# Optimization experiments

Hardware: AMD Instinct MI355X
Metric: run time of the kernel (lower is better)

Reference implementation:

```python
import jax, jax.numpy as jnp
import numpy as np

D = 1024          # embeddings_dims
HS = 128          # head_size = D // no_of_q_heads(=8)
NKV = 2           # hardcoded self.no_of_kv_heads = 2 (number of query Linear layers)


def apply_rope(x):
    # x: [..., T, d]; pairs of adjacent elements rotated (faithful to RotaryEmbeddings)
    d = x.shape[-1]
    T = x.shape[-2]
    positions = jnp.arange(0, d, 2, dtype=jnp.float32)           # step-2 positions (as in source)
    theta = 10000.0 ** (-2.0 * positions / d)                    # [d/2]
    angles = jnp.arange(T, dtype=jnp.float32)[:, None] * theta[None, :]  # [T, d/2]
    cos, sin = jnp.cos(angles), jnp.sin(angles)
    xr = x.reshape(x.shape[:-1] + (d // 2, 2))
    out = jnp.stack([xr[..., 0] * cos - xr[..., 1] * sin,
                     xr[..., 1] * cos + xr[..., 0] * sin], axis=-1)
    return out.reshape(x.shape)


def setup_inputs() -> dict:
    key = jax.random.key(0)
    k1, k2, k3, k4, k5 = jax.random.split(key, 5)
    B, T = 4, 2048
    x = jax.random.normal(k1, (B, T, D), dtype=jnp.float32)
    s = 1.0 / np.sqrt(D)
    Wq = jax.random.normal(k2, (NKV, HS, D), dtype=jnp.float32) * s  # 2 query Linear layers [out,in]
    Wk = jax.random.normal(k3, (HS, D), dtype=jnp.float32) * s
    Wv = jax.random.normal(k4, (HS, D), dtype=jnp.float32) * s
    Wo = jax.random.normal(k5, (D, NKV * HS), dtype=jnp.float32) * (1.0 / np.sqrt(NKV * HS))
    return {"x": x, "Wq": Wq, "Wk": Wk, "Wv": Wv, "Wo": Wo}


def reference(x, Wq, Wk, Wv, Wo):
    B, T, _ = x.shape
    k = apply_rope(x @ Wk.T)                              # [B,T,HS]
    v = x @ Wv.T                                          # [B,T,HS]
    q = jnp.einsum('btd,hkd->bhtk', x, Wq)                # [B,2,T,HS]
    q = apply_rope(q)
    scale = HS ** (-0.5)
    scores = jnp.einsum('bhtk,bsk->bhts', q, k) * scale   # [B,2,T,T]
    causal = jnp.tril(jnp.ones((T, T), dtype=bool))
    scores = jnp.where(causal, scores, -jnp.inf)
    w = jax.nn.softmax(scores, axis=-1)                   # dropout is identity at eval
    out = jnp.einsum('bhts,bsk->bhtk', w, v)              # [B,2,T,HS]
    out = out.transpose(0, 2, 1, 3).reshape(B, T, NKV * HS)  # concat heads on last dim
    return out @ Wo.T                                     # [B,T,D]
```

## Files before the change

### kernel.cpp

```cpp
#include <hip/hip_runtime.h>
#include <math.h>

#define DD 1024
#define HSZ 128
#define NB 4
#define TT 2048

typedef __attribute__((ext_vector_type(8))) short bf16x8;
typedef __attribute__((ext_vector_type(4))) float f32x4;

typedef __attribute__((address_space(3))) unsigned int lds_u32_t;
typedef __attribute__((address_space(1))) unsigned int glb_u32_t;

__device__ inline void gll16(const void* g, void* l) {
    __builtin_amdgcn_global_load_lds((const glb_u32_t*)g, (lds_u32_t*)l, 16, 0, 0);
}

__device__ inline unsigned short f2bf(float f){
    unsigned u = __builtin_bit_cast(unsigned, f);
    u += 0x7fff + ((u >> 16) & 1);
    return (unsigned short)(u >> 16);
}

__global__ __launch_bounds__(256) void prep_kernel(
    const float* __restrict__ Wq, const float* __restrict__ Wk,
    const float* __restrict__ Wv, const float* __restrict__ Wo,
    unsigned short* __restrict__ Wbp, unsigned short* __restrict__ Wop,
    float2* __restrict__ tab)
{
    int bid = blockIdx.x, tid = threadIdx.x;
    if (bid < 512) {
        int i = bid * 256 + tid;
        int t = i >> 6, j = i & 63;
        float theta = __powf(10000.f, -(float)j * (1.f / 32.f));
        float ang = (float)t * theta;
        tab[i] = make_float2(__cosf(ang), __sinf(ang));
        return;
    }
    const float* s;
    unsigned short* dst;
    if (bid < 768) {
        int gc = (bid - 512) * 256 + tid;
        int tileid = gc >> 10;
        int ct = tileid >> 4, kk = tileid & 15;
        int ch = gc & 1023;
        int ns = ch >> 7, kc = (ch >> 6) & 1, l6 = ch & 63;
        int wrow = ct * 128 + ns * 16 + (l6 & 15);
        int kcol = kk * 64 + kc * 32 + (l6 >> 4) * 8;
        s = (wrow < 256) ? Wq + (size_t)wrow * DD
          : (wrow < 384) ? Wk + (size_t)(wrow - 256) * DD
                         : Wv + (size_t)(wrow - 384) * DD;
        s += kcol;
        dst = Wbp + (size_t)gc * 8;
    } else {
        int gc = (bid - 768) * 256 + tid;
        int tileid = gc >> 10;
        int ct = tileid >> 2, kk = tileid & 3;
        int ch = gc & 1023;
        int ns = ch >> 7, kc = (ch >> 6) & 1, l6 = ch & 63;
        int orow = ct * 128 + ns * 16 + (l6 & 15);
        int kcol = kk * 64 + kc * 32 + (l6 >> 4) * 8;
        s = Wo + (size_t)orow * 256 + kcol;
        dst = Wop + (size_t)gc * 8;
    }
    float4 a = ((const float4*)s)[0];
    float4 c = ((const float4*)s)[1];
    unsigned short o[8] = {f2bf(a.x),f2bf(a.y),f2bf(a.z),f2bf(a.w),
                           f2bf(c.x),f2bf(c.y),f2bf(c.z),f2bf(c.w)};
    *(uint4*)dst = *(const uint4*)o;
}

__global__ __launch_bounds__(256) void qkv_gemm_kernel(
    const float* __restrict__ x,
    const unsigned short* __restrict__ Wbp,
    const float2* __restrict__ tab,
    unsigned short* __restrict__ qo,
    unsigned short* __restrict__ Kp,
    unsigned short* __restrict__ Vp)
{
    int bid = blockIdx.x;
    int rt = bid & 127, ct = bid >> 7;
    int row0 = rt * 64;
    int b = row0 >> 11, t0 = row0 & (TT - 1);
    int tid = threadIdx.x;
    int wave = tid >> 6, lane = tid & 63;
    int mrow = lane & 15, quad = lane >> 4;

    __shared__ unsigned short Bs[2][8192];

    f32x4 acc[8];
    #pragma unroll
    for (int ns = 0; ns < 8; ++ns)
        #pragma unroll
        for (int r = 0; r < 4; ++r) acc[ns][r] = 0.f;

    const float* xrow = x + (size_t)(row0 + wave * 16 + mrow) * DD;

    {
        const unsigned short* wt = Wbp + (size_t)(ct * 16) * 8192;
        #pragma unroll
        for (int u = 0; u < 4; ++u)
            gll16(wt + (size_t)(u * 256 + tid) * 8, &Bs[0][(u * 256 + (tid & 192)) * 8]);
    }

    for (int kk = 0; kk < 16; ++kk) {
        __syncthreads();
        if (kk < 15) {
            const unsigned short* wt = Wbp + (size_t)(ct * 16 + kk + 1) * 8192;
            #pragma unroll
            for (int u = 0; u < 4; ++u)
                gll16(wt + (size_t)(u * 256 + tid) * 8, &Bs[(kk + 1) & 1][(u * 256 + (tid & 192)) * 8]);
        }
        bf16x8 af[2];
        #pragma unroll
        for (int kc = 0; kc < 2; ++kc) {
            const float* s = xrow + kk * 64 + kc * 32 + quad * 8;
            float4 f0 = ((const float4*)s)[0];
            float4 f1 = ((const float4*)s)[1];
            bf16x8 pk;
            pk[0]=(short)f2bf(f0.x); pk[1]=(short)f2bf(f0.y); pk[2]=(short)f2bf(f0.z); pk[3]=(short)f2bf(f0.w);
            pk[4]=(short)f2bf(f1.x); pk[5]=(short)f2bf(f1.y); pk[6]=(short)f2bf(f1.z); pk[7]=(short)f2bf(f1.w);
            af[kc] = pk;
        }
        const unsigned short* Bcur = Bs[kk & 1];
        #pragma unroll
        for (int kc = 0; kc < 2; ++kc)
            #pragma unroll
            for (int ns = 0; ns < 8; ++ns) {
                bf16x8 bb = *(const bf16x8*)(Bcur + ((ns * 2 + kc) * 64 + lane) * 8);
                acc[ns] = __builtin_amdgcn_mfma_f32_16x16x32_bf16(af[kc], bb, acc[ns], 0, 0, 0);
            }
    }

    __syncthreads();

    if (ct < 2) {
        unsigned short* dst = qo + (size_t)(b * 2 + ct) * TT * HSZ;
        #pragma unroll
        for (int ns = 0; ns < 8; ++ns) {
            int colloc = ns * 16 + mrow;
            int pj = colloc >> 1;
            #pragma unroll
            for (int r = 0; r < 4; ++r) {
                int t = t0 + wave * 16 + quad * 4 + r;
                float v = acc[ns][r];
                float vp = __shfl_xor(v, 1, 64);
                float2 cs = tab[t * 64 + pj];
                float outv = ((mrow & 1) == 0) ? (v * cs.x - vp * cs.y)
                                               : (v * cs.x + vp * cs.y);
                dst[(size_t)t * HSZ + colloc] = f2bf(outv);
            }
        }
    } else if (ct == 2) {
        unsigned short* A_ = (unsigned short*)Bs;
        #pragma unroll
        for (int ns = 0; ns < 8; ++ns) {
            int colloc = ns * 16 + mrow;
            int pj = colloc >> 1;
            int chunk = (ns >> 1) * 4 + wave;
            int lph = (ns & 1) * 2 + (mrow >> 3);
            #pragma unroll
            for (int r = 0; r < 4; ++r) {
                int t = t0 + wave * 16 + quad * 4 + r;
                float v = acc[ns][r];
                float vp = __shfl_xor(v, 1, 64);
                float2 cs = tab[t * 64 + pj];
                float outv = ((mrow & 1) == 0) ? (v * cs.x - vp * cs.y)
                                               : (v * cs.x + vp * cs.y);
                A_[chunk * 512 + (lph * 16 + quad * 4 + r) * 8 + (mrow & 7)] = f2bf(outv);
            }
        }
        __syncthreads();
        unsigned short* kd = Kp + (size_t)(b * 32 + (t0 >> 6)) * 8192;
        #pragma unroll
        for (int u = 0; u < 4; ++u)
            *(uint4*)(kd + (u * 256 + tid) * 8) = *(const uint4*)(A_ + (u * 256 + tid) * 8);
    } else {
        unsigned short* A_ = (unsigned short*)Bs;
        #pragma unroll
        for (int ns = 0; ns < 8; ++ns) {
            int chunk = ns * 2 + (wave >> 1);
            int lanep = ((wave & 1) * 2 + (quad >> 1)) * 16 + mrow;
            #pragma unroll
            for (int r = 0; r < 4; ++r)
                A_[chunk * 512 + lanep * 8 + (quad & 1) * 4 + r] = f2bf(acc[ns][r]);
        }
        __syncthreads();
        unsigned short* vd = Vp + (size_t)(b * 32 + (t0 >> 6)) * 8192;
        #pragma unroll
        for (int u = 0; u < 4; ++u)
            *(uint4*)(vd + (u * 256 + tid) * 8) = *(const uint4*)(A_ + (u * 256 + tid) * 8);
    }
}

__global__ __launch_bounds__(256, 2) void attn_mfma_kernel(
    const unsigned short* __restrict__ q,
    const unsigned short* __restrict__ Kp,
    const unsigned short* __restrict__ Vp,
    unsigned short* __restrict__ att)
{
    int bid = blockIdx.x;
    int qt = 63 - (bid >> 3);
    int bh = bid & 7;
    int b = bh >> 1, h = bh & 1;
    int q0 = qt * 32;
    int tid = threadIdx.x;
    int wave = tid >> 6, lane = tid & 63;
    int mrow = lane & 15, quad = lane >> 4;

    __shared__ char raw[66304];
    unsigned short* Psb = (unsigned short*)raw;
    float* Os  = (float*)(raw + 16384);
    float* Ms_ = (float*)(raw + 65536);
    float* Ls_ = Ms_ + 96;

    const unsigned short* qbase = q + (((size_t)(b * 2 + h)) * TT + q0 + mrow) * HSZ + quad * 8;
    bf16x8 qf[2][4];
    #pragma unroll
    for (int u = 0; u < 2; ++u)
        #pragma unroll
        for (int c = 0; c < 4; ++c)
            qf[u][c] = *(const bf16x8*)(qbase + u * 16 * HSZ + 32 * c);

    float mrun[2][4], lrun[2][4];
    f32x4 O[2][8];
    #pragma unroll
    for (int u = 0; u < 2; ++u) {
        #pragma unroll
        for (int r = 0; r < 4; ++r) { mrun[u][r] = -1e30f; lrun[u][r] = 0.f; }
        #pragma unroll
        for (int g = 0; g < 8; ++g)
            #pragma unroll
            for (int r = 0; r < 4; ++r) O[u][g][r] = 0.f;
    }

    const int NT = (qt >> 1) + 1;
    const float scl = 0.08838834764831845f;
    unsigned short* Pw = Psb + wave * 2048;

    for (int j = wave; j < NT; j += 4) {
        const unsigned short* Kt = Kp + (size_t)(b * 32 + j) * 8192;
        const unsigned short* Vt = Vp + (size_t)(b * 32 + j) * 8192;
        int s0 = j * 64;

        f32x4 S[2][4];
        #pragma unroll
        for (int u = 0; u < 2; ++u)
            #pragma unroll
            for (int f = 0; f < 4; ++f)
                #pragma unroll
                for (int r = 0; r < 4; ++r) S[u][f][r] = 0.f;

        #pragma unroll
        for (int c = 0; c < 4; ++c)
            #pragma unroll
            for (int f = 0; f < 4; ++f) {
                bf16x8 bk = *(const bf16x8*)(Kt + ((c * 4 + f) * 64 + lane) * 8);
                S[0][f] = __builtin_amdgcn_mfma_f32_16x16x32_bf16(qf[0][c], bk, S[0][f], 0, 0, 0);
                S[1][f] = __builtin_amdgcn_mfma_f32_16x16x32_bf16(qf[1][c], bk, S[1][f], 0, 0, 0);
            }

        if (j == NT - 1) {
            #pragma unroll
            for (int u = 0; u < 2; ++u)
                #pragma unroll
                for (int f = 0; f < 4; ++f) {
                    int sg = s0 + 16 * f + mrow;
                    #pragma unroll
                    for (int r = 0; r < 4; ++r) {
                        int qg = q0 + u * 16 + quad * 4 + r;
                        S[u][f][r] = (sg <= qg) ? S[u][f][r] * scl : -1e30f;
                    }
                }
        } else {
            #pragma unroll
            for (int u = 0; u < 2; ++u)
                #pragma unroll
                for (int f = 0; f < 4; ++f)
                    #pragma unroll
                    for (int r = 0; r < 4; ++r) S[u][f][r] *= scl;
        }

        #pragma unroll
        for (int u = 0; u < 2; ++u) {
            float al[4];
            #pragma unroll
            for (int r = 0; r < 4; ++r) {
                float v = fmaxf(fmaxf(S[u][0][r], S[u][1][r]), fmaxf(S[u][2][r], S[u][3][r]));
                v = fmaxf(v, __shfl_xor(v, 1, 64));
                v = fmaxf(v, __shfl_xor(v, 2, 64));
                v = fmaxf(v, __shfl_xor(v, 4, 64));
                v = fmaxf(v, __shfl_xor(v, 8, 64));
                float mn = fmaxf(mrun[u][r], v);
                al[r] = __expf(mrun[u][r] - mn);
                mrun[u][r] = mn;
            }
            #pragma unroll
            for (int f = 0; f < 4; ++f)
                #pragma unroll
                for (int r = 0; r < 4; ++r)
                    S[u][f][r] = __expf(S[u][f][r] - mrun[u][r]);
            #pragma unroll
            for (int r = 0; r < 4; ++r) {
                float v = (S[u][0][r] + S[u][1][r]) + (S[u][2][r] + S[u][3][r]);
                v += __shfl_xor(v, 1, 64);
                v += __shfl_xor(v, 2, 64);
                v += __shfl_xor(v, 4, 64);
                v += __shfl_xor(v, 8, 64);
                lrun[u][r] = lrun[u][r] * al[r] + v;
            }
            #pragma unroll
            for (int g = 0; g < 8; ++g) {
                O[u][g][0] *= al[0]; O[u][g][1] *= al[1];
                O[u][g][2] *= al[2]; O[u][g][3] *= al[3];
            }
            #pragma unroll
            for (int f = 0; f < 4; ++f) {
                int p = f >> 1;
                int hi2 = (2 * f + (mrow >> 3)) & 3;
                int jlo = mrow & 7;
                #pragma unroll
                for (int r = 0; r < 4; ++r)
                    Pw[u * 1024 + (p * 64 + hi2 * 16 + quad * 4 + r) * 8 + jlo] = f2bf(S[u][f][r]);
            }
        }

        bf16x8 pa[2][2];
        #pragma unroll
        for (int u = 0; u < 2; ++u)
            #pragma unroll
            for (int p = 0; p < 2; ++p)
                pa[u][p] = *(const bf16x8*)(Pw + u * 1024 + (p * 64 + lane) * 8);

        #pragma unroll
        for (int g = 0; g < 8; ++g)
            #pragma unroll
            for (int p = 0; p < 2; ++p) {
                bf16x8 bv = *(const bf16x8*)(Vt + ((g * 2 + p) * 64 + lane) * 8);
                O[0][g] = __builtin_amdgcn_mfma_f32_16x16x32_bf16(pa[0][p], bv, O[0][g], 0, 0, 0);
                O[1][g] = __builtin_amdgcn_mfma_f32_16x16x32_bf16(pa[1][p], bv, O[1][g], 0, 0, 0);
            }
    }

    if (wave) {
        float* Ow = Os + (wave - 1) * 4096;
        #pragma unroll
        for (int u = 0; u < 2; ++u)
            #pragma unroll
            for (int g = 0; g < 8; ++g)
                #pragma unroll
                for (int r = 0; r < 4; ++r)
                    Ow[(u * 16 + quad * 4 + r) * 128 + g * 16 + mrow] = O[u][g][r];
        if (mrow == 0) {
            #pragma unroll
            for (int u = 0; u < 2; ++u)
                #pragma unroll
                for (int r = 0; r < 4; ++r) {
                    Ms_[(wave - 1) * 32 + u * 16 + quad * 4 + r] = mrun[u][r];
                    Ls_[(wave - 1) * 32 + u * 16 + quad * 4 + r] = lrun[u][r];
                }
        }
    }
    __syncthreads();
    if (wave == 0) {
        unsigned short* ab = att + (((size_t)b * TT + q0) * 2 + h) * 128;
        #pragma unroll
        for (int u = 0; u < 2; ++u) {
            float a0[4], a1[4], a2[4], a3[4], inv[4];
            #pragma unroll
            for (int r = 0; r < 4; ++r) {
                int row = u * 16 + quad * 4 + r;
                float m0 = mrun[u][r], l0 = lrun[u][r];
                float m1 = Ms_[row],      l1 = Ls_[row];
                float m2 = Ms_[32 + row], l2 = Ls_[32 + row];
                float m3 = Ms_[64 + row], l3 = Ls_[64 + row];
                float mM = fmaxf(fmaxf(m0, m1), fmaxf(m2, m3));
                a0[r] = __expf(m0 - mM); a1[r] = __expf(m1 - mM);
                a2[r] = __expf(m2 - mM); a3[r] = __expf(m3 - mM);
                inv[r] = 1.f / (l0 * a0[r] + l1 * a1[r] + l2 * a2[r] + l3 * a3[r]);
            }
            #pragma unroll
            for (int g = 0; g < 8; ++g)
                #pragma unroll
                for (int r = 0; r < 4; ++r) {
                    int row = u * 16 + quad * 4 + r;
                    float o = O[u][g][r] * a0[r]
                            + Os[row * 128 + g * 16 + mrow] * a1[r]
                            + Os[4096 + row * 128 + g * 16 + mrow] * a2[r]
                            + Os[8192 + row * 128 + g * 16 + mrow] * a3[r];
                    ab[(size_t)row * 256 + g * 16 + mrow] = f2bf(o * inv[r]);
                }
        }
    }
}

__global__ __launch_bounds__(256) void outproj_gemm_kernel(
    const unsigned short* __restrict__ attb,
    const unsigned short* __restrict__ Wop,
    float* __restrict__ y)
{
    int bid = blockIdx.x;
    int rt = bid & 127, ct = bid >> 7;
    int row0 = rt * 64;
    int tid = threadIdx.x;
    int wave = tid >> 6, lane = tid & 63;
    int mrow = lane & 15, quad = lane >> 4;

    __shared__ unsigned short Bs[2][8192];

    f32x4 acc[8];
    #pragma unroll
    for (int ns = 0; ns < 8; ++ns)
        #pragma unroll
        for (int r = 0; r < 4; ++r) acc[ns][r] = 0.f;

    const unsigned short* arow = attb + (size_t)(row0 + wave * 16 + mrow) * 256;

    {
        const unsigned short* wt = Wop + (size_t)(ct * 4) * 8192;
        #pragma unroll
        for (int u = 0; u < 4; ++u)
            gll16(wt + (size_t)(u * 256 + tid) * 8, &Bs[0][(u * 256 + (tid & 192)) * 8]);
    }

    for (int kk = 0; kk < 4; ++kk) {
        __syncthreads();
        if (kk < 3) {
            const unsigned short* wt = Wop + (size_t)(ct * 4 + kk + 1) * 8192;
            #pragma unroll
            for (int u = 0; u < 4; ++u)
                gll16(wt + (size_t)(u * 256 + tid) * 8, &Bs[(kk + 1) & 1][(u * 256 + (tid & 192)) * 8]);
        }
        const unsigned short* Bcur = Bs[kk & 1];
        #pragma unroll
        for (int kc = 0; kc < 2; ++kc) {
            bf16x8 af = *(const bf16x8*)(arow + kk * 64 + kc * 32 + quad * 8);
            #pragma unroll
            for (int ns = 0; ns < 8; ++ns) {
                bf16x8 bb = *(const bf16x8*)(Bcur + ((ns * 2 + kc) * 64 + lane) * 8);
                acc[ns] = __builtin_amdgcn_mfma_f32_16x16x32_bf16(af, bb, acc[ns], 0, 0, 0);
            }
        }
    }

    #pragma unroll
    for (int ns = 0; ns < 8; ++ns)
        #pragma unroll
        for (int r = 0; r < 4; ++r) {
            int row = row0 + wave * 16 + quad * 4 + r;
            y[(size_t)row * DD + ct * 128 + ns * 16 + mrow] = acc[ns][r];
        }
}

extern "C" void kernel_launch(void* const* d_in, const int* in_sizes, int n_in,
                              void* d_out, int out_size, void* d_ws, size_t ws_size,
                              hipStream_t stream) {
    const float* x  = (const float*)d_in[0];
    const float* Wq = (const float*)d_in[1];
    const float* Wk = (const float*)d_in[2];
    const float* Wv = (const float*)d_in[3];
    const float* Wo = (const float*)d_in[4];
    float* y = (float*)d_out;

    char* ws = (char*)d_ws;
    unsigned short* at  = (unsigned short*)(ws);
    unsigned short* qo  = (unsigned short*)(ws + 4u  * 1024 * 1024);
    unsigned short* Kp  = (unsigned short*)(ws + 8u  * 1024 * 1024);
    unsigned short* Vp  = (unsigned short*)(ws + 10u * 1024 * 1024);
    unsigned short* Wbp = (unsigned short*)(ws + 12u * 1024 * 1024);
    unsigned short* Wop = (unsigned short*)(ws + 13u * 1024 * 1024);
    float2*         tb  = (float2*)        (ws + 13824u * 1024);

    prep_kernel<<<896, 256, 0, stream>>>(Wq, Wk, Wv, Wo, Wbp, Wop, tb);
    qkv_gemm_kernel<<<512, 256, 0, stream>>>(x, Wbp, tb, qo, Kp, Vp);
    attn_mfma_kernel<<<512, 256, 0, stream>>>(qo, Kp, Vp, at);
    outproj_gemm_kernel<<<1024, 256, 0, stream>>>(at, Wop, y);
}
```

Before: 159.4 us.

## Pre-convert x to bf16, fold softmax scale into Q, MFMA row sums, swizzle P

Several changes land together. When the workspace is large enough, x is converted once to bf16 in the prep kernel, so the QKV GEMM loads bf16 fragments instead of converting fp32 in every column tile. The softmax scale is folded into the Q store, and the per-row sum is computed with an MFMA against a ones vector instead of shuffle reductions. P writes and reads in LDS get an XOR swizzle to reduce bank conflicts, and s_setprio is raised around the MFMA blocks. The trade-offs are an extra pass over x through memory and a small precision change, since the row sum now uses bf16-rounded P.

```diff
diff --git a/kernel.cpp b/kernel.cpp
--- a/kernel.cpp
+++ b/kernel.cpp
@@ -22,13 +22,25 @@
     return (unsigned short)(u >> 16);
 }
 
+#define QSCL 0.08838834764831845f
+
 __global__ __launch_bounds__(256) void prep_kernel(
     const float* __restrict__ Wq, const float* __restrict__ Wk,
     const float* __restrict__ Wv, const float* __restrict__ Wo,
     unsigned short* __restrict__ Wbp, unsigned short* __restrict__ Wop,
-    float2* __restrict__ tab)
+    float2* __restrict__ tab,
+    const float* __restrict__ x, unsigned short* __restrict__ xb)
 {
     int bid = blockIdx.x, tid = threadIdx.x;
+    if (bid >= 896) {
+        size_t i = (size_t)(bid - 896) * 256 + tid;
+        const float4* s = (const float4*)(x + i * 8);
+        float4 a = s[0], c = s[1];
+        unsigned short o[8] = {f2bf(a.x),f2bf(a.y),f2bf(a.z),f2bf(a.w),
+                               f2bf(c.x),f2bf(c.y),f2bf(c.z),f2bf(c.w)};
+        *(uint4*)(xb + i * 8) = *(const uint4*)o;
+        return;
+    }
     if (bid < 512) {
         int i = bid * 256 + tid;
         int t = i >> 6, j = i & 63;
@@ -70,8 +82,10 @@
     *(uint4*)dst = *(const uint4*)o;
 }
 
+template<bool XB>
 __global__ __launch_bounds__(256) void qkv_gemm_kernel(
     const float* __restrict__ x,
+    const unsigned short* __restrict__ xb,
     const unsigned short* __restrict__ Wbp,
     const float2* __restrict__ tab,
     unsigned short* __restrict__ qo,
@@ -95,6 +109,7 @@
         for (int r = 0; r < 4; ++r) acc[ns][r] = 0.f;
 
     const float* xrow = x + (size_t)(row0 + wave * 16 + mrow) * DD;
+    const unsigned short* xbrow = xb + (size_t)(row0 + wave * 16 + mrow) * DD;
 
     {
         const unsigned short* wt = Wbp + (size_t)(ct * 16) * 8192;
@@ -112,15 +127,20 @@
                 gll16(wt + (size_t)(u * 256 + tid) * 8, &Bs[(kk + 1) & 1][(u * 256 + (tid & 192)) * 8]);
         }
         bf16x8 af[2];
-        #pragma unroll
-        for (int kc = 0; kc < 2; ++kc) {
-            const float* s = xrow + kk * 64 + kc * 32 + quad * 8;
-            float4 f0 = ((const float4*)s)[0];
-            float4 f1 = ((const float4*)s)[1];
-            bf16x8 pk;
-            pk[0]=(short)f2bf(f0.x); pk[1]=(short)f2bf(f0.y); pk[2]=(short)f2bf(f0.z); pk[3]=(short)f2bf(f0.w);
-            pk[4]=(short)f2bf(f1.x); pk[5]=(short)f2bf(f1.y); pk[6]=(short)f2bf(f1.z); pk[7]=(short)f2bf(f1.w);
-            af[kc] = pk;
+        if (XB) {
+            af[0] = *(const bf16x8*)(xbrow + kk * 64 + quad * 8);
+            af[1] = *(const bf16x8*)(xbrow + kk * 64 + 32 + quad * 8);
+        } else {
+            #pragma unroll
+            for (int kc = 0; kc < 2; ++kc) {
+                const float* s = xrow + kk * 64 + kc * 32 + quad * 8;
+                float4 f0 = ((const float4*)s)[0];
+                float4 f1 = ((const float4*)s)[1];
+                bf16x8 pk;
+                pk[0]=(short)f2bf(f0.x); pk[1]=(short)f2bf(f0.y); pk[2]=(short)f2bf(f0.z); pk[3]=(short)f2bf(f0.w);
+                pk[4]=(short)f2bf(f1.x); pk[5]=(short)f2bf(f1.y); pk[6]=(short)f2bf(f1.z); pk[7]=(short)f2bf(f1.w);
+                af[kc] = pk;
+            }
         }
         const unsigned short* Bcur = Bs[kk & 1];
         #pragma unroll
@@ -148,7 +168,7 @@
                 float2 cs = tab[t * 64 + pj];
                 float outv = ((mrow & 1) == 0) ? (v * cs.x - vp * cs.y)
                                                : (v * cs.x + vp * cs.y);
-                dst[(size_t)t * HSZ + colloc] = f2bf(outv);
+                dst[(size_t)t * HSZ + colloc] = f2bf(outv * QSCL);
             }
         }
     } else if (ct == 2) {
@@ -222,12 +242,17 @@
         for (int c = 0; c < 4; ++c)
             qf[u][c] = *(const bf16x8*)(qbase + u * 16 * HSZ + 32 * c);
 
-    float mrun[2][4], lrun[2][4];
+    bf16x8 onesb;
+    #pragma unroll
+    for (int e = 0; e < 8; ++e) onesb[e] = (short)0x3F80;
+
+    float mrun[2][4];
     f32x4 O[2][8];
+    f32x4 Ol[2];
     #pragma unroll
     for (int u = 0; u < 2; ++u) {
         #pragma unroll
-        for (int r = 0; r < 4; ++r) { mrun[u][r] = -1e30f; lrun[u][r] = 0.f; }
+        for (int r = 0; r < 4; ++r) { mrun[u][r] = -1e30f; Ol[u][r] = 0.f; }
         #pragma unroll
         for (int g = 0; g < 8; ++g)
             #pragma unroll
@@ -235,7 +260,6 @@
     }
 
     const int NT = (qt >> 1) + 1;
-    const float scl = 0.08838834764831845f;
     unsigned short* Pw = Psb + wave * 2048;
 
     for (int j = wave; j < NT; j += 4) {
@@ -251,6 +275,7 @@
                 #pragma unroll
                 for (int r = 0; r < 4; ++r) S[u][f][r] = 0.f;
 
+        __builtin_amdgcn_s_setprio(1);
         #pragma unroll
         for (int c = 0; c < 4; ++c)
             #pragma unroll
@@ -259,6 +284,7 @@
                 S[0][f] = __builtin_amdgcn_mfma_f32_16x16x32_bf16(qf[0][c], bk, S[0][f], 0, 0, 0);
                 S[1][f] = __builtin_amdgcn_mfma_f32_16x16x32_bf16(qf[1][c], bk, S[1][f], 0, 0, 0);
             }
+        __builtin_amdgcn_s_setprio(0);
 
         if (j == NT - 1) {
             #pragma unroll
@@ -269,16 +295,9 @@
                     #pragma unroll
                     for (int r = 0; r < 4; ++r) {
                         int qg = q0 + u * 16 + quad * 4 + r;
-                        S[u][f][r] = (sg <= qg) ? S[u][f][r] * scl : -1e30f;
+                        S[u][f][r] = (sg <= qg) ? S[u][f][r] : -1e30f;
                     }
                 }
-        } else {
-            #pragma unroll
-            for (int u = 0; u < 2; ++u)
-                #pragma unroll
-                for (int f = 0; f < 4; ++f)
-                    #pragma unroll
-                    for (int r = 0; r < 4; ++r) S[u][f][r] *= scl;
         }
 
         #pragma unroll
@@ -301,27 +320,22 @@
                 for (int r = 0; r < 4; ++r)
                     S[u][f][r] = __expf(S[u][f][r] - mrun[u][r]);
             #pragma unroll
-            for (int r = 0; r < 4; ++r) {
-                float v = (S[u][0][r] + S[u][1][r]) + (S[u][2][r] + S[u][3][r]);
-                v += __shfl_xor(v, 1, 64);
-                v += __shfl_xor(v, 2, 64);
-                v += __shfl_xor(v, 4, 64);
-                v += __shfl_xor(v, 8, 64);
-                lrun[u][r] = lrun[u][r] * al[r] + v;
-            }
-            #pragma unroll
             for (int g = 0; g < 8; ++g) {
                 O[u][g][0] *= al[0]; O[u][g][1] *= al[1];
                 O[u][g][2] *= al[2]; O[u][g][3] *= al[3];
             }
+            Ol[u][0] *= al[0]; Ol[u][1] *= al[1]; Ol[u][2] *= al[2]; Ol[u][3] *= al[3];
             #pragma unroll
             for (int f = 0; f < 4; ++f) {
                 int p = f >> 1;
                 int hi2 = (2 * f + (mrow >> 3)) & 3;
                 int jlo = mrow & 7;
-                #pragma unroll
-                for (int r = 0; r < 4; ++r)
-                    Pw[u * 1024 + (p * 64 + hi2 * 16 + quad * 4 + r) * 8 + jlo] = f2bf(S[u][f][r]);
+                int gx = (quad >> 1) | (hi2 << 1);
+                #pragma unroll
+                for (int r = 0; r < 4; ++r) {
+                    int idx = p * 64 + hi2 * 16 + quad * 4 + r;
+                    Pw[u * 1024 + (idx ^ gx) * 8 + jlo] = f2bf(S[u][f][r]);
+                }
             }
         }
 
@@ -329,9 +343,17 @@
         #pragma unroll
         for (int u = 0; u < 2; ++u)
             #pragma unroll
-            for (int p = 0; p < 2; ++p)
-                pa[u][p] = *(const bf16x8*)(Pw + u * 1024 + (p * 64 + lane) * 8);
-
+            for (int p = 0; p < 2; ++p) {
+                int li = p * 64 + lane;
+                int si = li ^ ((li >> 3) & 7);
+                pa[u][p] = *(const bf16x8*)(Pw + u * 1024 + si * 8);
+            }
+
+        __builtin_amdgcn_s_setprio(1);
+        Ol[0] = __builtin_amdgcn_mfma_f32_16x16x32_bf16(pa[0][0], onesb, Ol[0], 0, 0, 0);
+        Ol[0] = __builtin_amdgcn_mfma_f32_16x16x32_bf16(pa[0][1], onesb, Ol[0], 0, 0, 0);
+        Ol[1] = __builtin_amdgcn_mfma_f32_16x16x32_bf16(pa[1][0], onesb, Ol[1], 0, 0, 0);
+        Ol[1] = __builtin_amdgcn_mfma_f32_16x16x32_bf16(pa[1][1], onesb, Ol[1], 0, 0, 0);
         #pragma unroll
         for (int g = 0; g < 8; ++g)
             #pragma unroll
@@ -340,6 +362,7 @@
                 O[0][g] = __builtin_amdgcn_mfma_f32_16x16x32_bf16(pa[0][p], bv, O[0][g], 0, 0, 0);
                 O[1][g] = __builtin_amdgcn_mfma_f32_16x16x32_bf16(pa[1][p], bv, O[1][g], 0, 0, 0);
             }
+        __builtin_amdgcn_s_setprio(0);
     }
 
     if (wave) {
@@ -357,7 +380,7 @@
                 #pragma unroll
                 for (int r = 0; r < 4; ++r) {
                     Ms_[(wave - 1) * 32 + u * 16 + quad * 4 + r] = mrun[u][r];
-                    Ls_[(wave - 1) * 32 + u * 16 + quad * 4 + r] = lrun[u][r];
+                    Ls_[(wave - 1) * 32 + u * 16 + quad * 4 + r] = Ol[u][r];
                 }
         }
     }
@@ -370,7 +393,7 @@
             #pragma unroll
             for (int r = 0; r < 4; ++r) {
                 int row = u * 16 + quad * 4 + r;
-                float m0 = mrun[u][r], l0 = lrun[u][r];
+                float m0 = mrun[u][r], l0 = Ol[u][r];
                 float m1 = Ms_[row],      l1 = Ls_[row];
                 float m2 = Ms_[32 + row], l2 = Ls_[32 + row];
                 float m3 = Ms_[64 + row], l3 = Ls_[64 + row];
@@ -470,9 +493,17 @@
     unsigned short* Wbp = (unsigned short*)(ws + 12u * 1024 * 1024);
     unsigned short* Wop = (unsigned short*)(ws + 13u * 1024 * 1024);
     float2*         tb  = (float2*)        (ws + 13824u * 1024);
-
-    prep_kernel<<<896, 256, 0, stream>>>(Wq, Wk, Wv, Wo, Wbp, Wop, tb);
-    qkv_gemm_kernel<<<512, 256, 0, stream>>>(x, Wbp, tb, qo, Kp, Vp);
+    unsigned short* xb  = (unsigned short*)(ws + 14848u * 1024);
+
+    bool big = ws_size >= (31ull << 20);
+
+    if (big) {
+        prep_kernel<<<4992, 256, 0, stream>>>(Wq, Wk, Wv, Wo, Wbp, Wop, tb, x, xb);
+        qkv_gemm_kernel<true><<<512, 256, 0, stream>>>(x, xb, Wbp, tb, qo, Kp, Vp);
+    } else {
+        prep_kernel<<<896, 256, 0, stream>>>(Wq, Wk, Wv, Wo, Wbp, Wop, tb, x, xb);
+        qkv_gemm_kernel<false><<<512, 256, 0, stream>>>(x, xb, Wbp, tb, qo, Kp, Vp);
+    }
     attn_mfma_kernel<<<512, 256, 0, stream>>>(qo, Kp, Vp, at);
     outproj_gemm_kernel<<<1024, 256, 0, stream>>>(at, Wop, y);
 }
```

Measured after the change: 170.5 us. 7.0% more time.
